# Kernel optimization log

Hardware: AMD Instinct MI355X
Metric: run time of the kernel (lower is better)

The kernel has to match this reference:

```python
import jax, jax.numpy as jnp
import numpy as np

SCALE = 1.0
N_TOTAL, B, K, C = 131072, 8, 20, 96


def setup_inputs() -> dict:
    key = jax.random.key(0)
    k1, k2, k3 = jax.random.split(key, 3)
    feats = jax.random.normal(k1, (N_TOTAL, C), dtype=jnp.float32)
    probs = jax.random.normal(k2, (N_TOTAL, K), dtype=jnp.float32)
    batch_indices = jnp.sort(jax.random.randint(k3, (N_TOTAL,), 0, B))
    return {"feats": feats, "probs": probs, "batch_size": B,
            "batch_indices": batch_indices}


def reference(feats, probs, batch_size, batch_indices):
    # Per-segment (per scan in the batch), per-class softmax over points,
    # then soft-weighted aggregation of point features -> [B, K, C].
    scaled = SCALE * probs                                            # [N, K]
    seg_max = jax.ops.segment_max(scaled, batch_indices,
                                  num_segments=batch_size)            # [B, K]
    seg_max = jnp.where(jnp.isfinite(seg_max), seg_max, 0.0)
    ex = jnp.exp(scaled - seg_max[batch_indices])                     # [N, K]
    denom = jax.ops.segment_sum(ex, batch_indices,
                                num_segments=batch_size)              # [B, K]
    w = ex / denom[batch_indices]                                     # [N, K] softmax within segment
    # Mask weights per batch and contract points with a batched matmul.
    onehot = (batch_indices[None, :] == jnp.arange(batch_size)[:, None]
              ).astype(feats.dtype)                                   # [B, N]
    wb = onehot[:, :, None] * w[None, :, :]                           # [B, N, K]
    context = jnp.einsum('bnk,nc->bkc', wb, feats)                    # [B, K, C]
    return context
```

## Files before the change

### kernel.cpp

```cpp
#include <hip/hip_runtime.h>
#include <math.h>

#define N_TOTAL 131072
#define BB 8
#define KK 20
#define CC 96
#define LOG2E 1.4426950408889634f

#define GLDS(g, l) __builtin_amdgcn_global_load_lds( \
    (const __attribute__((address_space(1))) void*)(g), \
    (__attribute__((address_space(3))) void*)(l), 16, 0, 0)

#define GA 512
#define CHUNKA 256
#define THRA 320

__global__ __launch_bounds__(THRA) void seg_s_kernel(
    const float* __restrict__ probs, const int* __restrict__ bidx,
    float* __restrict__ sPartT) {
  __shared__ float ls[64][BB * KK];
  const int t = threadIdx.x;
  for (int i = t; i < 64 * BB * KK; i += THRA) ((float*)ls)[i] = 0.f;
  const int base = blockIdx.x * CHUNKA;
  const int b0 = bidx[base];
  const bool multi = b0 != bidx[base + CHUNKA - 1];
  __syncthreads();
  const int p0 = (4 * t) / 20;
  const int k0 = (4 * t) % 20;
  const float4* src = (const float4*)(probs + (size_t)base * KK);
  float s0 = 0.f, s1 = 0.f, s2 = 0.f, s3 = 0.f;
  if (!multi) {
    #pragma unroll
    for (int i = 0; i < 4; ++i) {
      const float4 v = src[t + i * THRA];
      s0 += exp2f(v.x * LOG2E); s1 += exp2f(v.y * LOG2E);
      s2 += exp2f(v.z * LOG2E); s3 += exp2f(v.w * LOG2E);
    }
    ls[p0][b0 * KK + k0]     = s0; ls[p0][b0 * KK + k0 + 1] = s1;
    ls[p0][b0 * KK + k0 + 2] = s2; ls[p0][b0 * KK + k0 + 3] = s3;
  } else {
    int cb = bidx[base + p0];
    #pragma unroll
    for (int i = 0; i < 4; ++i) {
      const float4 v = src[t + i * THRA];
      const int b = bidx[base + p0 + i * 64];
      if (b != cb) {
        ls[p0][cb * KK + k0]     = s0; ls[p0][cb * KK + k0 + 1] = s1;
        ls[p0][cb * KK + k0 + 2] = s2; ls[p0][cb * KK + k0 + 3] = s3;
        s0 = s1 = s2 = s3 = 0.f; cb = b;
      }
      s0 += exp2f(v.x * LOG2E); s1 += exp2f(v.y * LOG2E);
      s2 += exp2f(v.z * LOG2E); s3 += exp2f(v.w * LOG2E);
    }
    ls[p0][cb * KK + k0]     = s0; ls[p0][cb * KK + k0 + 1] = s1;
    ls[p0][cb * KK + k0 + 2] = s2; ls[p0][cb * KK + k0 + 3] = s3;
  }
  __syncthreads();
  if (t < BB * KK) {
    float S = 0.f;
    #pragma unroll
    for (int u = 0; u < 64; ++u) S += ls[u][t];
    sPartT[(size_t)t * GA + blockIdx.x] = S;
  }
}

__global__ __launch_bounds__(256) void seg_off_kernel(
    const float* __restrict__ sPartT, float* __restrict__ off) {
  const int lane = threadIdx.x & 63;
  const int cl = threadIdx.x >> 6;
  const int cell = blockIdx.x * 4 + cl;
  const float* sp = sPartT + (size_t)cell * GA;
  float S = 0.f;
  #pragma unroll
  for (int i = 0; i < GA / 64; ++i) S += sp[lane + i * 64];
  #pragma unroll
  for (int d = 1; d < 64; d <<= 1) S += __shfl_xor(S, d);
  if (lane == 0) off[cell] = (S > 0.f) ? log2f(S) : 3e38f;
}

#define GC 512
#define THRC 256
#define CHK 64
#define NCH 4
#define BPTS (NCH * CHK)
#define FN (CHK * CC)
#define PN (CHK * KK)
#define BUFN (FN + PN)

__global__ __launch_bounds__(THRC) void gather_kernel(
    const float* __restrict__ feats, const float* __restrict__ probs,
    const int* __restrict__ bidx, const float* __restrict__ off,
    float* __restrict__ out, float* __restrict__ part, int useRed) {
  __shared__ float buf[2 * BUFN];
  __shared__ float loff[BB * KK];
  __shared__ float lacc[KK * CC];
  const int t = threadIdx.x;
  const int base = blockIdx.x * BPTS;
  const int b0 = bidx[base];
  const bool multi = b0 != bidx[base + BPTS - 1];

  if (t < BB * KK) loff[t] = off[t];
  for (int i = t; i < KK * CC; i += THRC) lacc[i] = 0.f;

  const bool active = t < 240;
  const int pslot = t / 60, r = t % 60;
  const int kg = r / 12, cg = r % 12;
  int cb = multi ? bidx[base + pslot * 16] : b0;

  asm volatile("s_waitcnt vmcnt(0)" ::: "memory");

  #define STAGE(g, h) {                                                      \
    const float* fsrc = feats + (size_t)(base + (g) * CHK) * CC;             \
    float* fb = buf + (h) * BUFN;                                            \
    _Pragma("unroll")                                                        \
    for (int i = 0; i < 6; ++i)                                              \
      GLDS(fsrc + (size_t)(i * THRC + t) * 4,                                \
           fb + (size_t)(i * THRC + (t & ~63)) * 4);                         \
    const float* psrc = probs + (size_t)(base + (g) * CHK) * KK;             \
    GLDS(psrc + (size_t)t * 4, fb + FN + (size_t)(t & ~63) * 4);             \
    if (t < 64) GLDS(psrc + (size_t)(256 + t) * 4, fb + FN + 1024);          \
  }

  STAGE(0, 0);

  float acc[4][8];
  #pragma unroll
  for (int i = 0; i < 4; ++i)
    #pragma unroll
    for (int j = 0; j < 8; ++j) acc[i][j] = 0.f;

  for (int g = 0; g < NCH; ++g) {
    if (g + 1 < NCH) {
      STAGE(g + 1, (g + 1) & 1);
      asm volatile("s_waitcnt vmcnt(7)" ::: "memory");
    } else {
      asm volatile("s_waitcnt vmcnt(0)" ::: "memory");
    }
    __builtin_amdgcn_s_barrier();
    __builtin_amdgcn_sched_barrier(0);

    const float* fb = buf + (g & 1) * BUFN;
    const float* pb = fb + FN;
    if (active) {
      float offr[4];
      #pragma unroll
      for (int i = 0; i < 4; ++i) offr[i] = loff[cb * KK + kg * 4 + i];
      const float* wp = pb + (size_t)(pslot * 16) * KK + kg * 4;
      const float* f1 = fb + (size_t)(pslot * 16) * CC + cg * 4;
      const float* f2 = f1 + 48;
      #pragma unroll 2
      for (int pass = 0; pass < 16; ++pass) {
        if (multi) {
          const int b = bidx[base + g * CHK + pslot * 16 + pass];
          if (b != cb) {
            #pragma unroll
            for (int i = 0; i < 4; ++i)
              #pragma unroll
              for (int j = 0; j < 8; ++j) {
                const int c = (j < 4) ? cg * 4 + j : 48 + cg * 4 + (j - 4);
                atomicAdd(out + cb * (KK * CC) + (kg * 4 + i) * CC + c, acc[i][j]);
                acc[i][j] = 0.f;
              }
            cb = b;
            #pragma unroll
            for (int i = 0; i < 4; ++i) offr[i] = loff[cb * KK + kg * 4 + i];
          }
        }
        const float4 w4 = *(const float4*)(wp + pass * KK);
        const float4 fA = *(const float4*)(f1 + (size_t)pass * CC);
        const float4 fB = *(const float4*)(f2 + (size_t)pass * CC);
        float wr[4];
        wr[0] = exp2f(fmaf(w4.x, LOG2E, -offr[0]));
        wr[1] = exp2f(fmaf(w4.y, LOG2E, -offr[1]));
        wr[2] = exp2f(fmaf(w4.z, LOG2E, -offr[2]));
        wr[3] = exp2f(fmaf(w4.w, LOG2E, -offr[3]));
        const float fr[8] = {fA.x, fA.y, fA.z, fA.w, fB.x, fB.y, fB.z, fB.w};
        #pragma unroll
        for (int i = 0; i < 4; ++i)
          #pragma unroll
          for (int j = 0; j < 8; ++j)
            acc[i][j] = fmaf(wr[i], fr[j], acc[i][j]);
      }
    }
    asm volatile("s_waitcnt lgkmcnt(0)" ::: "memory");
    __builtin_amdgcn_s_barrier();
    __builtin_amdgcn_sched_barrier(0);
  }

  if (active) {
    if (multi) {
      #pragma unroll
      for (int i = 0; i < 4; ++i)
        #pragma unroll
        for (int j = 0; j < 8; ++j) {
          const int c = (j < 4) ? cg * 4 + j : 48 + cg * 4 + (j - 4);
          atomicAdd(out + cb * (KK * CC) + (kg * 4 + i) * CC + c, acc[i][j]);
        }
    } else {
      #pragma unroll
      for (int i = 0; i < 4; ++i)
        #pragma unroll
        for (int j = 0; j < 8; ++j) {
          const int c = (j < 4) ? cg * 4 + j : 48 + cg * 4 + (j - 4);
          atomicAdd(&lacc[(kg * 4 + i) * CC + c], acc[i][j]);
        }
    }
  }
  __syncthreads();
  if (!multi) {
    if (useRed) {
      for (int i = t; i < KK * CC; i += THRC)
        part[(size_t)blockIdx.x * (KK * CC) + i] = lacc[i];
    } else {
      for (int i = t; i < KK * CC; i += THRC)
        atomicAdd(out + (size_t)b0 * (KK * CC) + i, lacc[i]);
    }
  }
}

#define RGB 16
#define RCB 8
__global__ __launch_bounds__(256) void reduce_kernel(
    const float* __restrict__ part, const int* __restrict__ bidx,
    float* __restrict__ out) {
  const int gblk = blockIdx.x / RCB;
  const int cblk = blockIdx.x % RCB;
  const int t = threadIdx.x;
  if (t >= 240) return;
  const int c = cblk * 240 + t;
  float acc = 0.f; int cb = -1;
  const int g0 = gblk * (GC / RGB);
  for (int g = g0; g < g0 + GC / RGB; ++g) {
    const int bA = bidx[g * BPTS];
    if (bA != bidx[g * BPTS + BPTS - 1]) continue;
    if (bA != cb) {
      if (cb >= 0) atomicAdd(out + (size_t)cb * (KK * CC) + c, acc);
      acc = 0.f; cb = bA;
    }
    acc += part[(size_t)g * (KK * CC) + c];
  }
  if (cb >= 0) atomicAdd(out + (size_t)cb * (KK * CC) + c, acc);
}

extern "C" void kernel_launch(void* const* d_in, const int* in_sizes, int n_in,
                              void* d_out, int out_size, void* d_ws, size_t ws_size,
                              hipStream_t stream) {
  const float* feats = (const float*)d_in[0];
  const float* probs = (const float*)d_in[1];
  const int* bidx = (const int*)d_in[3];
  float* out = (float*)d_out;

  float* sPartT = (float*)d_ws;
  float* off    = sPartT + (size_t)BB * KK * GA;
  float* part   = off + BB * KK;
  const size_t need = ((size_t)BB * KK * GA + BB * KK +
                       (size_t)GC * KK * CC) * sizeof(float);
  const int useRed = ws_size >= need;

  hipMemsetAsync(d_out, 0, (size_t)BB * KK * CC * sizeof(float), stream);
  seg_s_kernel<<<GA, THRA, 0, stream>>>(probs, bidx, sPartT);
  seg_off_kernel<<<BB * KK / 4, 256, 0, stream>>>(sPartT, off);
  gather_kernel<<<GC, THRC, 0, stream>>>(feats, probs, bidx, off, out, part, useRed);
  if (useRed)
    reduce_kernel<<<RGB * RCB, 256, 0, stream>>>(part, bidx, out);
}
```

Baseline: 147.6 us.

## Fuse all stages into one cooperative kernel with grid-wide syncs

Replaces the memset and the four separate launches (segment sums, offsets, gather, reduce) with a single cooperative persistent kernel that separates the phases with grid syncs. Each block recomputes the log-sum offsets it needs instead of reading them from a separate kernel. Blocks grow to 512 threads, with each thread covering 8 points per chunk instead of 16. The aim is to remove launch gaps and inter-kernel overheads, at the cost of grid-sync latency, redundant offset computation per block and a serial final reduction loop over 512 partials.

Result: slower. 271.7 us (+84.2%).

```diff
diff --git a/kernel.cpp b/kernel.cpp
--- a/kernel.cpp
+++ b/kernel.cpp
@@ -1,245 +1,258 @@
 #include <hip/hip_runtime.h>
+#include <hip/hip_cooperative_groups.h>
 #include <math.h>
 
-#define N_TOTAL 131072
+namespace cg = cooperative_groups;
+
 #define BB 8
 #define KK 20
 #define CC 96
 #define LOG2E 1.4426950408889634f
 
+#define VB   512
+#define THR  512
+#define BPTS 256
+#define CHK  64
+#define NCH  4
+#define FN   (CHK * CC)
+#define PN   (CHK * KK)
+#define BUFN (FN + PN)
+
 #define GLDS(g, l) __builtin_amdgcn_global_load_lds( \
     (const __attribute__((address_space(1))) void*)(g), \
     (__attribute__((address_space(3))) void*)(l), 16, 0, 0)
 
-#define GA 512
-#define CHUNKA 256
-#define THRA 320
-
-__global__ __launch_bounds__(THRA) void seg_s_kernel(
-    const float* __restrict__ probs, const int* __restrict__ bidx,
-    float* __restrict__ sPartT) {
-  __shared__ float ls[64][BB * KK];
-  const int t = threadIdx.x;
-  for (int i = t; i < 64 * BB * KK; i += THRA) ((float*)ls)[i] = 0.f;
-  const int base = blockIdx.x * CHUNKA;
-  const int b0 = bidx[base];
-  const bool multi = b0 != bidx[base + CHUNKA - 1];
-  __syncthreads();
-  const int p0 = (4 * t) / 20;
-  const int k0 = (4 * t) % 20;
-  const float4* src = (const float4*)(probs + (size_t)base * KK);
-  float s0 = 0.f, s1 = 0.f, s2 = 0.f, s3 = 0.f;
-  if (!multi) {
-    #pragma unroll
-    for (int i = 0; i < 4; ++i) {
-      const float4 v = src[t + i * THRA];
-      s0 += exp2f(v.x * LOG2E); s1 += exp2f(v.y * LOG2E);
-      s2 += exp2f(v.z * LOG2E); s3 += exp2f(v.w * LOG2E);
-    }
-    ls[p0][b0 * KK + k0]     = s0; ls[p0][b0 * KK + k0 + 1] = s1;
-    ls[p0][b0 * KK + k0 + 2] = s2; ls[p0][b0 * KK + k0 + 3] = s3;
-  } else {
-    int cb = bidx[base + p0];
-    #pragma unroll
-    for (int i = 0; i < 4; ++i) {
-      const float4 v = src[t + i * THRA];
-      const int b = bidx[base + p0 + i * 64];
-      if (b != cb) {
-        ls[p0][cb * KK + k0]     = s0; ls[p0][cb * KK + k0 + 1] = s1;
-        ls[p0][cb * KK + k0 + 2] = s2; ls[p0][cb * KK + k0 + 3] = s3;
-        s0 = s1 = s2 = s3 = 0.f; cb = b;
-      }
-      s0 += exp2f(v.x * LOG2E); s1 += exp2f(v.y * LOG2E);
-      s2 += exp2f(v.z * LOG2E); s3 += exp2f(v.w * LOG2E);
-    }
-    ls[p0][cb * KK + k0]     = s0; ls[p0][cb * KK + k0 + 1] = s1;
-    ls[p0][cb * KK + k0 + 2] = s2; ls[p0][cb * KK + k0 + 3] = s3;
-  }
-  __syncthreads();
-  if (t < BB * KK) {
-    float S = 0.f;
-    #pragma unroll
-    for (int u = 0; u < 64; ++u) S += ls[u][t];
-    sPartT[(size_t)t * GA + blockIdx.x] = S;
-  }
-}
-
-__global__ __launch_bounds__(256) void seg_off_kernel(
-    const float* __restrict__ sPartT, float* __restrict__ off) {
-  const int lane = threadIdx.x & 63;
-  const int cl = threadIdx.x >> 6;
-  const int cell = blockIdx.x * 4 + cl;
-  const float* sp = sPartT + (size_t)cell * GA;
-  float S = 0.f;
-  #pragma unroll
-  for (int i = 0; i < GA / 64; ++i) S += sp[lane + i * 64];
-  #pragma unroll
-  for (int d = 1; d < 64; d <<= 1) S += __shfl_xor(S, d);
-  if (lane == 0) off[cell] = (S > 0.f) ? log2f(S) : 3e38f;
-}
-
-#define GC 512
-#define THRC 256
-#define CHK 64
-#define NCH 4
-#define BPTS (NCH * CHK)
-#define FN (CHK * CC)
-#define PN (CHK * KK)
-#define BUFN (FN + PN)
-
-__global__ __launch_bounds__(THRC) void gather_kernel(
-    const float* __restrict__ feats, const float* __restrict__ probs,
-    const int* __restrict__ bidx, const float* __restrict__ off,
-    float* __restrict__ out, float* __restrict__ part, int useRed) {
-  __shared__ float buf[2 * BUFN];
+#define STAGE(g, h) {                                                       \
+    const float* fsrc_ = feats + (size_t)(base + (g) * CHK) * CC;           \
+    float* fb_ = buf + (h) * BUFN;                                          \
+    _Pragma("unroll")                                                       \
+    for (int i_ = 0; i_ < 3; ++i_)                                          \
+      GLDS(fsrc_ + (size_t)(i_ * THR + t) * 4,                              \
+           fb_ + (size_t)(i_ * THR + (t & ~63)) * 4);                       \
+    const float* psrc_ = probs + (size_t)(base + (g) * CHK) * KK;           \
+    if (t < 320)                                                            \
+      GLDS(psrc_ + (size_t)t * 4, fb_ + FN + (size_t)(t & ~63) * 4);        \
+  }
+
+__launch_bounds__(THR, 4)
+__global__ void fused_kernel(const float* __restrict__ feats,
+                             const float* __restrict__ probs,
+                             const int* __restrict__ bidx,
+                             float* __restrict__ out,
+                             float* __restrict__ sPartT,
+                             float* __restrict__ part,
+                             int useRed) {
+  __shared__ __align__(16) float buf[2 * BUFN];
   __shared__ float loff[BB * KK];
   __shared__ float lacc[KK * CC];
   const int t = threadIdx.x;
-  const int base = blockIdx.x * BPTS;
-  const int b0 = bidx[base];
-  const bool multi = b0 != bidx[base + BPTS - 1];
-
-  if (t < BB * KK) loff[t] = off[t];
-  for (int i = t; i < KK * CC; i += THRC) lacc[i] = 0.f;
-
-  const bool active = t < 240;
-  const int pslot = t / 60, r = t % 60;
-  const int kg = r / 12, cg = r % 12;
-  int cb = multi ? bidx[base + pslot * 16] : b0;
-
-  asm volatile("s_waitcnt vmcnt(0)" ::: "memory");
-
-  #define STAGE(g, h) {                                                      \
-    const float* fsrc = feats + (size_t)(base + (g) * CHK) * CC;             \
-    float* fb = buf + (h) * BUFN;                                            \
-    _Pragma("unroll")                                                        \
-    for (int i = 0; i < 6; ++i)                                              \
-      GLDS(fsrc + (size_t)(i * THRC + t) * 4,                                \
-           fb + (size_t)(i * THRC + (t & ~63)) * 4);                         \
-    const float* psrc = probs + (size_t)(base + (g) * CHK) * KK;             \
-    GLDS(psrc + (size_t)t * 4, fb + FN + (size_t)(t & ~63) * 4);             \
-    if (t < 64) GLDS(psrc + (size_t)(256 + t) * 4, fb + FN + 1024);          \
-  }
-
-  STAGE(0, 0);
-
-  float acc[4][8];
-  #pragma unroll
-  for (int i = 0; i < 4; ++i)
+  const int nb = gridDim.x;
+  cg::grid_group gg = cg::this_grid();
+
+  if (blockIdx.x == 0)
+    for (int i = t; i < BB * KK * CC; i += THR) out[i] = 0.f;
+  float* ls = buf;
+  for (int vb = blockIdx.x; vb < VB; vb += nb) {
+    const int base = vb * BPTS;
+    const int b0 = bidx[base];
+    const bool multi = b0 != bidx[base + BPTS - 1];
+    for (int i = t; i < 64 * BB * KK; i += THR) ls[i] = 0.f;
+    __syncthreads();
+    if (t < 320) {
+      const int p0 = (4 * t) / 20;
+      const int k0 = (4 * t) % 20;
+      const float4* src = (const float4*)(probs + (size_t)base * KK);
+      float s0 = 0.f, s1 = 0.f, s2 = 0.f, s3 = 0.f;
+      if (!multi) {
+        #pragma unroll
+        for (int i = 0; i < 4; ++i) {
+          const float4 v = src[t + i * 320];
+          s0 += exp2f(v.x * LOG2E); s1 += exp2f(v.y * LOG2E);
+          s2 += exp2f(v.z * LOG2E); s3 += exp2f(v.w * LOG2E);
+        }
+        float* c = &ls[p0 * (BB * KK) + b0 * KK + k0];
+        c[0] = s0; c[1] = s1; c[2] = s2; c[3] = s3;
+      } else {
+        int cb = bidx[base + p0];
+        #pragma unroll
+        for (int i = 0; i < 4; ++i) {
+          const float4 v = src[t + i * 320];
+          const int b = bidx[base + p0 + i * 64];
+          if (b != cb) {
+            float* c = &ls[p0 * (BB * KK) + cb * KK + k0];
+            c[0] = s0; c[1] = s1; c[2] = s2; c[3] = s3;
+            s0 = s1 = s2 = s3 = 0.f; cb = b;
+          }
+          s0 += exp2f(v.x * LOG2E); s1 += exp2f(v.y * LOG2E);
+          s2 += exp2f(v.z * LOG2E); s3 += exp2f(v.w * LOG2E);
+        }
+        float* c = &ls[p0 * (BB * KK) + cb * KK + k0];
+        c[0] = s0; c[1] = s1; c[2] = s2; c[3] = s3;
+      }
+    }
+    __syncthreads();
+    if (t < BB * KK) {
+      float S = 0.f;
+      #pragma unroll
+      for (int u = 0; u < 64; ++u) S += ls[u * (BB * KK) + t];
+      sPartT[(size_t)t * VB + vb] = S;
+    }
+    __syncthreads();
+  }
+  gg.sync();
+
+  for (int vb = blockIdx.x; vb < VB; vb += nb) {
+    const int base = vb * BPTS;
+    const int b0 = bidx[base];
+    const int bL = bidx[base + BPTS - 1];
+    const bool multi = b0 != bL;
+    for (int bb = b0; bb <= bL; ++bb) {
+      #pragma unroll
+      for (int cq = 0; cq < 3; ++cq) {
+        const int k = cq * 8 + (t >> 6);
+        if (k < 20) {
+          const float* sp = sPartT + (size_t)(bb * KK + k) * VB;
+          float S = 0.f;
+          #pragma unroll
+          for (int i = 0; i < 8; ++i) S += sp[(t & 63) + i * 64];
+          #pragma unroll
+          for (int d = 1; d < 64; d <<= 1) S += __shfl_xor(S, d);
+          if ((t & 63) == 0) loff[bb * KK + k] = (S > 0.f) ? log2f(S) : 3e38f;
+        }
+      }
+    }
+    for (int i = t; i < KK * CC; i += THR) lacc[i] = 0.f;
+
+    const bool act = t < 480;
+    const int pslot = t / 60, r = t % 60;
+    const int kg = r / 12, cg = r % 12;
+    int cb = b0;
+    if (act && multi) cb = bidx[base + pslot * 8];
+    asm volatile("s_waitcnt vmcnt(0)" ::: "memory");
+    __syncthreads();
+
+    float offr[4];
+    if (act) {
+      #pragma unroll
+      for (int i = 0; i < 4; ++i) offr[i] = loff[cb * KK + kg * 4 + i];
+    }
+    float acc[4][8];
     #pragma unroll
-    for (int j = 0; j < 8; ++j) acc[i][j] = 0.f;
-
-  for (int g = 0; g < NCH; ++g) {
-    if (g + 1 < NCH) {
-      STAGE(g + 1, (g + 1) & 1);
-      asm volatile("s_waitcnt vmcnt(7)" ::: "memory");
-    } else {
-      asm volatile("s_waitcnt vmcnt(0)" ::: "memory");
-    }
-    __builtin_amdgcn_s_barrier();
-    __builtin_amdgcn_sched_barrier(0);
-
-    const float* fb = buf + (g & 1) * BUFN;
-    const float* pb = fb + FN;
-    if (active) {
-      float offr[4];
-      #pragma unroll
-      for (int i = 0; i < 4; ++i) offr[i] = loff[cb * KK + kg * 4 + i];
-      const float* wp = pb + (size_t)(pslot * 16) * KK + kg * 4;
-      const float* f1 = fb + (size_t)(pslot * 16) * CC + cg * 4;
-      const float* f2 = f1 + 48;
-      #pragma unroll 2
-      for (int pass = 0; pass < 16; ++pass) {
-        if (multi) {
-          const int b = bidx[base + g * CHK + pslot * 16 + pass];
-          if (b != cb) {
+    for (int i = 0; i < 4; ++i)
+      #pragma unroll
+      for (int j = 0; j < 8; ++j) acc[i][j] = 0.f;
+
+    STAGE(0, 0);
+    for (int g = 0; g < NCH; ++g) {
+      if (g + 1 < NCH) {
+        STAGE(g + 1, (g + 1) & 1);
+        asm volatile("s_waitcnt vmcnt(3)" ::: "memory");
+      } else {
+        asm volatile("s_waitcnt vmcnt(0)" ::: "memory");
+      }
+      __builtin_amdgcn_s_barrier();
+      __builtin_amdgcn_sched_barrier(0);
+
+      const float* fb = buf + (g & 1) * BUFN;
+      const float* pb = fb + FN;
+      if (act) {
+        const float* wp = pb + (pslot * 8) * KK + kg * 4;
+        const float* f1 = fb + (size_t)(pslot * 8) * CC + cg * 4;
+        const float* f2 = f1 + 48;
+        #pragma unroll 4
+        for (int pass = 0; pass < 8; ++pass) {
+          if (multi) {
+            const int b = bidx[base + g * CHK + pslot * 8 + pass];
+            if (b != cb) {
+              #pragma unroll
+              for (int i = 0; i < 4; ++i)
+                #pragma unroll
+                for (int j = 0; j < 8; ++j) {
+                  const int c = (j < 4) ? cg * 4 + j : 48 + cg * 4 + (j - 4);
+                  atomicAdd(out + (size_t)cb * (KK * CC) + (kg * 4 + i) * CC + c,
+                            acc[i][j]);
+                  acc[i][j] = 0.f;
+                }
+              cb = b;
+              #pragma unroll
+              for (int i = 0; i < 4; ++i) offr[i] = loff[cb * KK + kg * 4 + i];
+            }
+          }
+          const float4 w4 = *(const float4*)(wp + pass * KK);
+          const float4 fA = *(const float4*)(f1 + (size_t)pass * CC);
+          const float4 fB = *(const float4*)(f2 + (size_t)pass * CC);
+          float wr[4];
+          wr[0] = exp2f(fmaf(w4.x, LOG2E, -offr[0]));
+          wr[1] = exp2f(fmaf(w4.y, LOG2E, -offr[1]));
+          wr[2] = exp2f(fmaf(w4.z, LOG2E, -offr[2]));
+          wr[3] = exp2f(fmaf(w4.w, LOG2E, -offr[3]));
+          const float fr[8] = {fA.x, fA.y, fA.z, fA.w, fB.x, fB.y, fB.z, fB.w};
+          #pragma unroll
+          for (int i = 0; i < 4; ++i)
             #pragma unroll
-            for (int i = 0; i < 4; ++i)
-              #pragma unroll
-              for (int j = 0; j < 8; ++j) {
-                const int c = (j < 4) ? cg * 4 + j : 48 + cg * 4 + (j - 4);
-                atomicAdd(out + cb * (KK * CC) + (kg * 4 + i) * CC + c, acc[i][j]);
-                acc[i][j] = 0.f;
-              }
-            cb = b;
-            #pragma unroll
-            for (int i = 0; i < 4; ++i) offr[i] = loff[cb * KK + kg * 4 + i];
-          }
-        }
-        const float4 w4 = *(const float4*)(wp + pass * KK);
-        const float4 fA = *(const float4*)(f1 + (size_t)pass * CC);
-        const float4 fB = *(const float4*)(f2 + (size_t)pass * CC);
-        float wr[4];
-        wr[0] = exp2f(fmaf(w4.x, LOG2E, -offr[0]));
-        wr[1] = exp2f(fmaf(w4.y, LOG2E, -offr[1]));
-        wr[2] = exp2f(fmaf(w4.z, LOG2E, -offr[2]));
-        wr[3] = exp2f(fmaf(w4.w, LOG2E, -offr[3]));
-        const float fr[8] = {fA.x, fA.y, fA.z, fA.w, fB.x, fB.y, fB.z, fB.w};
+            for (int j = 0; j < 8; ++j)
+              acc[i][j] = fmaf(wr[i], fr[j], acc[i][j]);
+        }
+      }
+      asm volatile("s_waitcnt lgkmcnt(0)" ::: "memory");
+      __builtin_amdgcn_s_barrier();
+      __builtin_amdgcn_sched_barrier(0);
+    }
+
+    if (act) {
+      if (multi) {
         #pragma unroll
         for (int i = 0; i < 4; ++i)
           #pragma unroll
-          for (int j = 0; j < 8; ++j)
-            acc[i][j] = fmaf(wr[i], fr[j], acc[i][j]);
-      }
-    }
-    asm volatile("s_waitcnt lgkmcnt(0)" ::: "memory");
-    __builtin_amdgcn_s_barrier();
-    __builtin_amdgcn_sched_barrier(0);
-  }
-
-  if (active) {
-    if (multi) {
-      #pragma unroll
-      for (int i = 0; i < 4; ++i)
-        #pragma unroll
-        for (int j = 0; j < 8; ++j) {
-          const int c = (j < 4) ? cg * 4 + j : 48 + cg * 4 + (j - 4);
-          atomicAdd(out + cb * (KK * CC) + (kg * 4 + i) * CC + c, acc[i][j]);
-        }
-    } else {
-      #pragma unroll
-      for (int i = 0; i < 4; ++i)
-        #pragma unroll
-        for (int j = 0; j < 8; ++j) {
-          const int c = (j < 4) ? cg * 4 + j : 48 + cg * 4 + (j - 4);
-          atomicAdd(&lacc[(kg * 4 + i) * CC + c], acc[i][j]);
-        }
-    }
-  }
-  __syncthreads();
-  if (!multi) {
-    if (useRed) {
-      for (int i = t; i < KK * CC; i += THRC)
-        part[(size_t)blockIdx.x * (KK * CC) + i] = lacc[i];
-    } else {
-      for (int i = t; i < KK * CC; i += THRC)
-        atomicAdd(out + (size_t)b0 * (KK * CC) + i, lacc[i]);
-    }
-  }
-}
-
-#define RGB 16
-#define RCB 8
-__global__ __launch_bounds__(256) void reduce_kernel(
-    const float* __restrict__ part, const int* __restrict__ bidx,
-    float* __restrict__ out) {
-  const int gblk = blockIdx.x / RCB;
-  const int cblk = blockIdx.x % RCB;
-  const int t = threadIdx.x;
-  if (t >= 240) return;
-  const int c = cblk * 240 + t;
-  float acc = 0.f; int cb = -1;
-  const int g0 = gblk * (GC / RGB);
-  for (int g = g0; g < g0 + GC / RGB; ++g) {
-    const int bA = bidx[g * BPTS];
-    if (bA != bidx[g * BPTS + BPTS - 1]) continue;
-    if (bA != cb) {
-      if (cb >= 0) atomicAdd(out + (size_t)cb * (KK * CC) + c, acc);
-      acc = 0.f; cb = bA;
-    }
-    acc += part[(size_t)g * (KK * CC) + c];
-  }
-  if (cb >= 0) atomicAdd(out + (size_t)cb * (KK * CC) + c, acc);
+          for (int j = 0; j < 8; ++j) {
+            const int c = (j < 4) ? cg * 4 + j : 48 + cg * 4 + (j - 4);
+            atomicAdd(out + (size_t)cb * (KK * CC) + (kg * 4 + i) * CC + c,
+                      acc[i][j]);
+          }
+      } else {
+        #pragma unroll
+        for (int i = 0; i < 4; ++i)
+          #pragma unroll
+          for (int j = 0; j < 8; ++j) {
+            const int c = (j < 4) ? cg * 4 + j : 48 + cg * 4 + (j - 4);
+            atomicAdd(&lacc[(kg * 4 + i) * CC + c], acc[i][j]);
+          }
+      }
+    }
+    __syncthreads();
+    if (!multi) {
+      if (useRed) {
+        for (int i = t; i < KK * CC; i += THR)
+          part[(size_t)vb * (KK * CC) + i] = lacc[i];
+      } else {
+        for (int i = t; i < KK * CC; i += THR)
+          atomicAdd(out + (size_t)b0 * (KK * CC) + i, lacc[i]);
+      }
+    }
+    __syncthreads();
+  }
+  gg.sync();
+
+  if (useRed) {
+    for (int rb = blockIdx.x; rb < 64; rb += nb) {
+      const int b = rb >> 3, cs = rb & 7;
+      int* gb = (int*)lacc;
+      {
+        const int bA = bidx[t * BPTS];
+        gb[t] = (bA == bidx[t * BPTS + BPTS - 1]) ? bA : -1;
+      }
+      __syncthreads();
+      if (t < 240) {
+        const int c = cs * 240 + t;
+        float a = 0.f;
+        for (int g = 0; g < VB; ++g)
+          if (gb[g] == b)
+            a += part[(size_t)g * (KK * CC) + c];
+        atomicAdd(out + (size_t)b * (KK * CC) + c, a);
+      }
+      __syncthreads();
+    }
+  }
 }
 
 extern "C" void kernel_launch(void* const* d_in, const int* in_sizes, int n_in,
@@ -251,16 +264,19 @@
   float* out = (float*)d_out;
 
   float* sPartT = (float*)d_ws;
-  float* off    = sPartT + (size_t)BB * KK * GA;
-  float* part   = off + BB * KK;
-  const size_t need = ((size_t)BB * KK * GA + BB * KK +
-                       (size_t)GC * KK * CC) * sizeof(float);
-  const int useRed = ws_size >= need;
-
-  hipMemsetAsync(d_out, 0, (size_t)BB * KK * CC * sizeof(float), stream);
-  seg_s_kernel<<<GA, THRA, 0, stream>>>(probs, bidx, sPartT);
-  seg_off_kernel<<<BB * KK / 4, 256, 0, stream>>>(sPartT, off);
-  gather_kernel<<<GC, THRC, 0, stream>>>(feats, probs, bidx, off, out, part, useRed);
-  if (useRed)
-    reduce_kernel<<<RGB * RCB, 256, 0, stream>>>(part, bidx, out);
+  float* part = sPartT + (size_t)BB * KK * VB;
+  const size_t need = ((size_t)BB * KK * VB +
+                       (size_t)VB * KK * CC) * sizeof(float);
+  int useRed = ws_size >= need;
+
+  int occ = 1;
+  (void)hipOccupancyMaxActiveBlocksPerMultiprocessor(&occ, fused_kernel, THR, 0);
+  if (occ < 1) occ = 1;
+  if (occ > 2) occ = 2;
+  const int nb = 256 * occ;
+
+  void* args[] = {(void*)&feats, (void*)&probs, (void*)&bidx,
+                  (void*)&out, (void*)&sPartT, (void*)&part, (void*)&useRed};
+  hipLaunchCooperativeKernel((const void*)fused_kernel, dim3(nb), dim3(THR),
+                             args, 0, stream);
 }
```
